# Kernel optimization log

Measured on AMD Instinct MI355X. Metric: run time of the kernel, lower is better.

Reference implementation:

```python
import jax, jax.numpy as jnp
import numpy as np

B, T, D, H = 2, 2048, 1024, 16
HD = D // H
SCALE = HD ** -0.5
NEG_INF = float(np.finfo(np.float32).min)


def setup_inputs() -> dict:
    key = jax.random.key(0)
    ks = jax.random.split(key, 10)
    s = 1.0 / np.sqrt(D)
    x = jax.random.normal(ks[0], (B, T, D), dtype=jnp.float32)
    # causal mask, True = keep, shape (B,1,T,T)
    mask = jnp.broadcast_to(jnp.tril(jnp.ones((T, T), dtype=bool)), (B, 1, T, T))
    Wq = jax.random.normal(ks[1], (D, D), dtype=jnp.float32) * s
    bq = jax.random.normal(ks[2], (D,), dtype=jnp.float32) * s
    Wk = jax.random.normal(ks[3], (D, D), dtype=jnp.float32) * s
    bk = jax.random.normal(ks[4], (D,), dtype=jnp.float32) * s
    Wv = jax.random.normal(ks[5], (D, D), dtype=jnp.float32) * s
    bv = jax.random.normal(ks[6], (D,), dtype=jnp.float32) * s
    Wo = jax.random.normal(ks[7], (D, D), dtype=jnp.float32) * s
    bo = jax.random.normal(ks[8], (D,), dtype=jnp.float32) * s
    return {"x": x, "mask": mask, "Wq": Wq, "bq": bq, "Wk": Wk, "bk": bk,
            "Wv": Wv, "bv": bv, "Wo": Wo, "bo": bo}


def _split_heads(t):
    # (B,T,D) -> (B,H,T,HD)
    return t.reshape(B, T, H, HD).transpose(0, 2, 1, 3)


def masked_rowwise_softmax(scores, mask):
    # mask: bool, True = keep; fully-masked rows return zeros.
    s = scores.astype(jnp.float32)
    masked = jnp.where(mask, s, NEG_INF)
    row_max = jnp.max(masked, axis=-1, keepdims=True)
    exps = jnp.exp(masked - row_max) * mask.astype(jnp.float32)
    denom = jnp.maximum(jnp.sum(exps, axis=-1, keepdims=True), 1e-12)
    return (exps / denom).astype(scores.dtype)


def reference(x, mask, Wq, bq, Wk, bk, Wv, bv, Wo, bo):
    q = _split_heads(x @ Wq.T + bq)
    k = _split_heads(x @ Wk.T + bk)
    v = _split_heads(x @ Wv.T + bv)
    scores = jnp.einsum('bhqd,bhkd->bhqk', q, k) * SCALE
    m = jnp.broadcast_to(mask, (B, H, T, T))
    attn = masked_rowwise_softmax(scores, m)
    y = jnp.einsum('bhqk,bhkd->bhqd', attn, v)
    y = y.transpose(0, 2, 1, 3).reshape(B, T, D)
    return y @ Wo.T + bo
```

## Files before the change

### kernel.cpp

```cpp
#include <hip/hip_runtime.h>

#define B_ 2
#define H_ 16
#define T_ 2048
#define D_ 1024
#define HD_ 64
#define NEG_HUGE (-3.402823466e38f)
#define QSCALE 0.18033688011112042f

typedef unsigned short u16;
typedef unsigned int u32;
typedef __attribute__((ext_vector_type(8))) short bf16x8;
typedef __attribute__((ext_vector_type(4))) float f32x4;
typedef __attribute__((ext_vector_type(4))) u32 u32x4;

__device__ __forceinline__ u16 f2bf(float f) {
    u32 u = __builtin_bit_cast(u32, f);
    u += 0x7FFFu + ((u >> 16) & 1u);
    return (u16)(u >> 16);
}

__device__ __forceinline__ u32 pk2bf(float f0, float f1) {
    const u32 a0 = __builtin_bit_cast(u32, f0) + 0x8000u;
    const u32 a1 = __builtin_bit_cast(u32, f1) + 0x8000u;
    return __builtin_amdgcn_perm(a1, a0, 0x07060302u);
}

__device__ __forceinline__ uint2 pk4bf(f32x4 a) {
    uint2 r;
    r.x = pk2bf(a[0], a[1]);
    r.y = pk2bf(a[2], a[3]);
    return r;
}

__device__ __forceinline__ f32x4 mfma16(bf16x8 a, bf16x8 b, f32x4 c) {
    return __builtin_amdgcn_mfma_f32_16x16x32_bf16(a, b, c, 0, 0, 0);
}

__global__ __launch_bounds__(256) void to_bf16(
    const float* __restrict__ x,  const float* __restrict__ wq,
    const float* __restrict__ wk, const float* __restrict__ wv,
    const float* __restrict__ wo, u16* __restrict__ dst)
{
    const size_t g = ((size_t)blockIdx.x * 256 + threadIdx.x) * 8;
    const float* src; size_t off;
    if      (g < (size_t)(4u << 20)) { src = x;  off = g; }
    else if (g < (size_t)(5u << 20)) { src = wq; off = g - (size_t)(4u << 20); }
    else if (g < (size_t)(6u << 20)) { src = wk; off = g - (size_t)(5u << 20); }
    else if (g < (size_t)(7u << 20)) { src = wv; off = g - (size_t)(6u << 20); }
    else                             { src = wo; off = g - (size_t)(7u << 20); }
    const float4 a = *(const float4*)&src[off];
    const float4 b = *(const float4*)&src[off + 4];
    ushort4 lo = make_ushort4(f2bf(a.x), f2bf(a.y), f2bf(a.z), f2bf(a.w));
    ushort4 hi = make_ushort4(f2bf(b.x), f2bf(b.y), f2bf(b.z), f2bf(b.w));
    *(ushort4*)&dst[g]     = lo;
    *(ushort4*)&dst[g + 4] = hi;
}

__device__ __forceinline__ void gemm128_core(
    const u16* __restrict__ P0, const u16* __restrict__ P1,
    const int m0, const int n0, u16* As, u16* Bs, f32x4 (&acc)[4][4])
{
    const int tid  = threadIdx.x;
    const int lane = tid & 63;
    const int quad = lane >> 4;
    const int l15  = lane & 15;
    const int w    = tid >> 6;
    const int wm   = (w >> 1) << 6;
    const int wn   = (w & 1) << 6;
    const int swz  = l15 & 7;

    size_t aoff[4], boff[4];
    int    loff[4];
#pragma unroll
    for (int i = 0; i < 4; ++i) {
        const int slot = i * 256 + tid;
        const int r = slot >> 3, c = slot & 7;
        const int gc = (c ^ (r & 7)) << 3;
        aoff[i] = (size_t)(m0 + r) * D_ + gc;
        boff[i] = (size_t)(n0 + r) * D_ + gc;
        loff[i] = slot * 8;
    }
    int rowA[4], rowB[4];
#pragma unroll
    for (int i = 0; i < 4; ++i) {
        rowA[i] = (wm + i * 16 + l15) * 64;
        rowB[i] = (wn + i * 16 + l15) * 64;
    }

    bf16x8 pa[4], pb[4];
#pragma unroll
    for (int i = 0; i < 4; ++i) {
        pa[i] = *(const bf16x8*)&P0[aoff[i]];
        pb[i] = *(const bf16x8*)&P1[boff[i]];
    }

    for (int k0 = 0; k0 < D_; k0 += 64) {
        __syncthreads();
#pragma unroll
        for (int i = 0; i < 4; ++i) {
            *(bf16x8*)&As[loff[i]] = pa[i];
            *(bf16x8*)&Bs[loff[i]] = pb[i];
        }
        if (k0 + 64 < D_) {
            const int kn = k0 + 64;
#pragma unroll
            for (int i = 0; i < 4; ++i) {
                pa[i] = *(const bf16x8*)&P0[aoff[i] + kn];
                pb[i] = *(const bf16x8*)&P1[boff[i] + kn];
            }
        }
        __syncthreads();
#pragma unroll
        for (int s = 0; s < 2; ++s) {
            const int ch = (((s << 2) + quad) ^ swz) << 3;
            bf16x8 am[4], bm[4];
#pragma unroll
            for (int mi = 0; mi < 4; ++mi) am[mi] = *(const bf16x8*)&As[rowA[mi] + ch];
#pragma unroll
            for (int ni = 0; ni < 4; ++ni) bm[ni] = *(const bf16x8*)&Bs[rowB[ni] + ch];
#pragma unroll
            for (int mi = 0; mi < 4; ++mi)
#pragma unroll
                for (int ni = 0; ni < 4; ++ni)
                    acc[mi][ni] = mfma16(am[mi], bm[ni], acc[mi][ni]);
        }
    }
}

__global__ __launch_bounds__(256) void gemm_qkv(
    const u16* __restrict__ xb,
    const u16* __restrict__ Wqb, const u16* __restrict__ Wkb, const u16* __restrict__ Wvb,
    const float* __restrict__ bq, const float* __restrict__ bk, const float* __restrict__ bv,
    u16* __restrict__ Qb, u16* __restrict__ Kb, u16* __restrict__ Vtb)
{
    __shared__ u16 As[128 * 64];
    __shared__ u16 Bs[128 * 64];
    const int L   = blockIdx.x;
    const int xcd = L & 7;
    const int kk  = L >> 3;
    const int tt  = (xcd << 2) + (kk & 3);
    const int ft  = (kk >> 2) & 7;
    const int z   = kk >> 5;

    f32x4 acc[4][4];
#pragma unroll
    for (int i = 0; i < 4; ++i)
#pragma unroll
        for (int j = 0; j < 4; ++j) acc[i][j] = (f32x4){0.f, 0.f, 0.f, 0.f};

    const int tid  = threadIdx.x;
    const int lane = tid & 63;
    const int quad = lane >> 4;
    const int l15  = lane & 15;
    const int w    = tid >> 6;
    const int wm   = (w >> 1) << 6;
    const int wn   = (w & 1) << 6;
    const int pq   = quad >> 1;
    const int psub = (quad & 1) << 2;

    u16* scr = ((w < 2) ? As : Bs) + ((w & 1) ? 4096 : 0);

    if (z < 2) {
        const u16*   W    = z ? Wkb : Wqb;
        const float* bias = z ? bk  : bq;
        const float  CF   = z ? 1.f : QSCALE;
        u16*         C    = z ? Kb  : Qb;
        const int m0 = ft << 7;
        const int n0 = tt << 7;
        gemm128_core(W, xb, m0, n0, As, Bs, acc);
        __syncthreads();

        const int fb = m0 + wm;
        const int h  = fb >> 6;
        const int tb = n0 + wn;
#pragma unroll
        for (int i = 0; i < 4; ++i) {
            const float4 bi = *(const float4*)&bias[fb + i * 16 + (quad << 2)];
#pragma unroll
            for (int j = 0; j < 4; ++j) {
                const int tl = j * 16 + l15;
                f32x4 a = acc[i][j];
                f32x4 v = { (a[0] + bi.x) * CF, (a[1] + bi.y) * CF,
                            (a[2] + bi.z) * CF, (a[3] + bi.w) * CF };
                *(uint2*)&scr[tl * 64 + (((2 * i + pq) ^ (tl & 7)) << 3) + psub] = pk4bf(v);
            }
        }
        __asm__ volatile("s_waitcnt lgkmcnt(0)" ::: "memory");

        const int b  = tb >> 11;
        const int t0 = tb & 2047;
#pragma unroll
        for (int e = 0; e < 8; ++e) {
            const int tl = (lane >> 3) + e * 8;
            const int c  = lane & 7;
            bf16x8 v = *(const bf16x8*)&scr[tl * 64 + ((c ^ (tl & 7)) << 3)];
            *(bf16x8*)&C[((size_t)((b << 4) + h) * T_ + t0 + tl) * HD_ + (c << 3)] = v;
        }
    } else {
        const int m0 = tt << 7;
        const int n0 = ft << 7;
        gemm128_core(xb, Wvb, m0, n0, As, Bs, acc);
        __syncthreads();

#pragma unroll
        for (int j = 0; j < 4; ++j) {
            const int row = j * 16 + l15;
            const float bi = bv[n0 + wn + row];
            const int sw = row & 7;
#pragma unroll
            for (int i = 0; i < 4; ++i) {
                f32x4 a = acc[i][j];
                f32x4 v = { a[0] + bi, a[1] + bi, a[2] + bi, a[3] + bi };
                *(uint2*)&scr[row * 64 + (((2 * i + pq) ^ sw) << 3) + psub] = pk4bf(v);
            }
        }
        __asm__ volatile("s_waitcnt lgkmcnt(0)" ::: "memory");

        const int b  = (m0 + wm) >> 11;
        const int t0 = (m0 + wm) & 2047;
        const int h  = (n0 + wn) >> 6;
#pragma unroll
        for (int e = 0; e < 8; ++e) {
            const int hdl = (lane >> 3) + e * 8;
            const int c   = lane & 7;
            bf16x8 vv = *(const bf16x8*)&scr[hdl * 64 + ((c ^ (hdl & 7)) << 3)];
            *(bf16x8*)&Vtb[((size_t)((b << 4) + h) * HD_ + hdl) * T_ + t0 + (c << 3)] = vv;
        }
    }
}

__global__ __launch_bounds__(256) void gemm_out(
    const u16* __restrict__ Ab, const u16* __restrict__ Wob,
    const float* __restrict__ bo, float* __restrict__ C)
{
    __shared__ u16 As[128 * 64];
    __shared__ u16 Bs[128 * 64];
    const int L   = blockIdx.x;
    const int xcd = L & 7;
    const int kk  = L >> 3;
    const int tt  = (xcd << 2) + (kk & 3);
    const int ft  = kk >> 2;
    const int m0  = tt << 7;
    const int n0  = ft << 7;

    f32x4 acc[4][4];
#pragma unroll
    for (int i = 0; i < 4; ++i)
#pragma unroll
        for (int j = 0; j < 4; ++j) acc[i][j] = (f32x4){0.f, 0.f, 0.f, 0.f};

    gemm128_core(Ab, Wob, m0, n0, As, Bs, acc);

    const int tid  = threadIdx.x;
    const int lane = tid & 63;
    const int quad = lane >> 4;
    const int l15  = lane & 15;
    const int w    = tid >> 6;
    const int wm   = (w >> 1) << 6;
    const int wn   = (w & 1) << 6;

    float bi[4];
#pragma unroll
    for (int ni = 0; ni < 4; ++ni) bi[ni] = bo[n0 + wn + ni * 16 + l15];

#pragma unroll
    for (int mi = 0; mi < 4; ++mi) {
        const int m = m0 + wm + mi * 16 + (quad << 2);
#pragma unroll
        for (int r = 0; r < 4; ++r)
#pragma unroll
            for (int ni = 0; ni < 4; ++ni)
                C[(size_t)(m + r) * D_ + n0 + wn + ni * 16 + l15] = acc[mi][ni][r] + bi[ni];
    }
}

__global__ __launch_bounds__(256) void attn_mfma(
    const u16* __restrict__ Qg, const u16* __restrict__ Kg,
    const u16* __restrict__ Vtg, u16* __restrict__ Out)
{
    __shared__ u16 Ks[128 * 64];
    __shared__ u16 Vs[64 * 128];
    const int tid  = threadIdx.x;
    const int w    = tid >> 6;
    const int lane = tid & 63;
    const int quad = lane >> 4;
    const int l15  = lane & 15;
    const int bh   = blockIdx.x;
    const int qt   = 31 - (int)blockIdx.y;
    const size_t base = (size_t)bh * (T_ * HD_);

    int lK[4], lV[4];
    size_t gK[4], gV[4];
#pragma unroll
    for (int i = 0; i < 4; ++i) {
        const int slot = i * 256 + tid;
        const int rk = slot >> 3, ck = slot & 7;
        lK[i] = rk * 64 + ((ck ^ (rk & 7)) << 3);
        gK[i] = base + (size_t)rk * HD_ + ck * 8;
        const int rv = slot >> 4, cv = slot & 15;
        lV[i] = rv * 128 + ((cv ^ (rv & 15)) << 3);
        gV[i] = base + (size_t)rv * T_ + cv * 8;
    }

    bf16x8 ones;
#pragma unroll
    for (int i = 0; i < 8; ++i) ones[i] = (short)0x3F80;

    const int swz7 = l15 & 7;
    const int b = bh >> 4, h = bh & 15;

    const int qloc = (w << 4) + l15;
    const int qrow = (qt << 6) + qloc;
    const bf16x8 qf0 = *(const bf16x8*)&Qg[base + (size_t)qrow * HD_ + quad * 8];
    const bf16x8 qf1 = *(const bf16x8*)&Qg[base + (size_t)qrow * HD_ + 32 + quad * 8];

    f32x4 o[4];
#pragma unroll
    for (int nt = 0; nt < 4; ++nt) o[nt] = (f32x4){0.f, 0.f, 0.f, 0.f};
    f32x4 Lacc = (f32x4){0.f, 0.f, 0.f, 0.f};

    const int nIter = (qt + 2) >> 1;
    bf16x8 kreg[4], vreg[4];
#pragma unroll
    for (int i = 0; i < 4; ++i) {
        kreg[i] = *(const bf16x8*)&Kg[gK[i]];
        vreg[i] = *(const bf16x8*)&Vtg[gV[i]];
    }

    for (int it = 0; it < nIter; ++it) {
        __syncthreads();
#pragma unroll
        for (int i = 0; i < 4; ++i) {
            *(bf16x8*)&Ks[lK[i]] = kreg[i];
            *(bf16x8*)&Vs[lV[i]] = vreg[i];
        }
        if (it + 1 < nIter) {
            const int koff = (it + 1) << 7;
#pragma unroll
            for (int i = 0; i < 4; ++i) {
                kreg[i] = *(const bf16x8*)&Kg[gK[i] + (size_t)koff * HD_];
                vreg[i] = *(const bf16x8*)&Vtg[gV[i] + koff];
            }
        }
        __syncthreads();

        f32x4 st[8];
#pragma unroll
        for (int t = 0; t < 8; ++t) {
            const int kr = (t * 16 + l15) * 64;
            const bf16x8 k0 = *(const bf16x8*)&Ks[kr + ((quad ^ swz7) << 3)];
            const bf16x8 k1 = *(const bf16x8*)&Ks[kr + (((quad + 4) ^ swz7) << 3)];
            f32x4 a = (f32x4){0.f, 0.f, 0.f, 0.f};
            a = mfma16(k0, qf0, a);
            a = mfma16(k1, qf1, a);
            st[t] = a;
        }

        if (it == nIter - 1) {
            const int koff = it << 7;
#pragma unroll
            for (int t = 0; t < 8; ++t)
#pragma unroll
                for (int r = 0; r < 4; ++r) {
                    const int kg = koff + t * 16 + (quad << 2) + r;
                    if (kg > qrow) st[t][r] = NEG_HUGE;
                }
        }

#pragma unroll
        for (int t = 0; t < 8; ++t)
#pragma unroll
            for (int r = 0; r < 4; ++r) st[t][r] = __builtin_amdgcn_exp2f(st[t][r]);

        bf16x8 pf[4];
#pragma unroll
        for (int kq = 0; kq < 4; ++kq) {
            u32 c00 = pk2bf(st[2 * kq][0],     st[2 * kq][1]);
            u32 c01 = pk2bf(st[2 * kq][2],     st[2 * kq][3]);
            u32 c10 = pk2bf(st[2 * kq + 1][0], st[2 * kq + 1][1]);
            u32 c11 = pk2bf(st[2 * kq + 1][2], st[2 * kq + 1][3]);
            asm("v_permlane32_swap_b32 %0, %1" : "+v"(c00), "+v"(c10));
            asm("v_permlane16_swap_b32 %0, %1" : "+v"(c00), "+v"(c10));
            asm("v_permlane32_swap_b32 %0, %1" : "+v"(c01), "+v"(c11));
            asm("v_permlane16_swap_b32 %0, %1" : "+v"(c01), "+v"(c11));
            u32x4 dw;
            dw[0] = c00; dw[1] = c01; dw[2] = c10; dw[3] = c11;
            pf[kq] = __builtin_bit_cast(bf16x8, dw);
        }

        __builtin_amdgcn_s_setprio(1);
#pragma unroll
        for (int nt = 0; nt < 4; ++nt) {
            f32x4 oo = o[nt];
            const int vr = (nt * 16 + l15) * 128;
#pragma unroll
            for (int kq = 0; kq < 4; ++kq) {
                const bf16x8 vf = *(const bf16x8*)&Vs[vr + ((((kq << 2) + quad) ^ l15) << 3)];
                oo = mfma16(pf[kq], vf, oo);
            }
            o[nt] = oo;
        }
#pragma unroll
        for (int kq = 0; kq < 4; ++kq)
            Lacc = mfma16(pf[kq], ones, Lacc);
        __builtin_amdgcn_s_setprio(0);
    }

    f32x4 linv;
#pragma unroll
    for (int r = 0; r < 4; ++r) linv[r] = 1.f / fmaxf(Lacc[r], 1e-30f);

#pragma unroll
    for (int nt = 0; nt < 4; ++nt)
#pragma unroll
        for (int r = 0; r < 4; ++r) {
            const int qg2 = (qt << 6) + (w << 4) + (quad << 2) + r;
            const u32 u = __builtin_bit_cast(u32, o[nt][r] * linv[r]) + 0x8000u;
            Out[(size_t)(b * T_ + qg2) * D_ + (h << 6) + nt * 16 + l15] = (u16)(u >> 16);
        }
}

extern "C" void kernel_launch(void* const* d_in, const int* in_sizes, int n_in,
                              void* d_out, int out_size, void* d_ws, size_t ws_size,
                              hipStream_t stream)
{
    const float* x  = (const float*)d_in[0];
    const float* Wq = (const float*)d_in[2];
    const float* bq = (const float*)d_in[3];
    const float* Wk = (const float*)d_in[4];
    const float* bk = (const float*)d_in[5];
    const float* Wv = (const float*)d_in[6];
    const float* bv = (const float*)d_in[7];
    const float* Wo = (const float*)d_in[8];
    const float* bo = (const float*)d_in[9];
    float* out = (float*)d_out;

    const size_t M1 = (size_t)1 << 20;
    u16* wsu = (u16*)d_ws;
    u16* xb  = wsu;
    u16* wqb = wsu + 4 * M1;
    u16* wkb = wsu + 5 * M1;
    u16* wvb = wsu + 6 * M1;
    u16* wob = wsu + 7 * M1;
    u16* Qb  = wsu + 8 * M1;
    u16* Kb  = wsu + 12 * M1;
    u16* Vtb = wsu + 16 * M1;
    u16* AOb = wsu + 20 * M1;

    to_bf16<<<4096, 256, 0, stream>>>(x, Wq, Wk, Wv, Wo, wsu);

    gemm_qkv<<<768, 256, 0, stream>>>(xb, wqb, wkb, wvb, bq, bk, bv, Qb, Kb, Vtb);

    dim3 ga(B_ * H_, T_ / 64);
    attn_mfma<<<ga, 256, 0, stream>>>(Qb, Kb, Vtb, AOb);

    gemm_out<<<256, 256, 0, stream>>>(AOb, wob, bo, out);
}
```

Measured before the change: 188.6 us.

## Rewrite QKV GEMM with 256x256 tiles, direct-to-LDS loads and double buffering

The QKV projection kernel now uses 512-thread blocks computing 256x256 output tiles (192 blocks instead of 768), with each wave owning a 128x64 sub-tile. Operands are streamed straight into LDS via global_load_lds in a two-stage double-buffered pipeline, with setprio around MFMA bursts and explicit barriers and waitcnts. The epilogues are rewritten for the wider tiles. The aim is more data reuse per byte loaded and overlap of loads with compute, at the cost of 128 KB of LDS, higher register pressure and fewer blocks than CUs, which may leave some CUs idle.

```diff
diff --git a/kernel.cpp b/kernel.cpp
--- a/kernel.cpp
+++ b/kernel.cpp
@@ -13,6 +13,9 @@
 typedef __attribute__((ext_vector_type(8))) short bf16x8;
 typedef __attribute__((ext_vector_type(4))) float f32x4;
 typedef __attribute__((ext_vector_type(4))) u32 u32x4;
+
+typedef const __attribute__((address_space(1))) void* gas_t;
+typedef __attribute__((address_space(3))) void* las_t;
 
 __device__ __forceinline__ u16 f2bf(float f) {
     u32 u = __builtin_bit_cast(u32, f);
@@ -128,104 +131,183 @@
     }
 }
 
-__global__ __launch_bounds__(256) void gemm_qkv(
+__global__ __launch_bounds__(512, 2) void gemm_qkv(
     const u16* __restrict__ xb,
     const u16* __restrict__ Wqb, const u16* __restrict__ Wkb, const u16* __restrict__ Wvb,
     const float* __restrict__ bq, const float* __restrict__ bk, const float* __restrict__ bv,
     u16* __restrict__ Qb, u16* __restrict__ Kb, u16* __restrict__ Vtb)
 {
-    __shared__ u16 As[128 * 64];
-    __shared__ u16 Bs[128 * 64];
-    const int L   = blockIdx.x;
-    const int xcd = L & 7;
-    const int kk  = L >> 3;
-    const int tt  = (xcd << 2) + (kk & 3);
-    const int ft  = (kk >> 2) & 7;
-    const int z   = kk >> 5;
-
-    f32x4 acc[4][4];
-#pragma unroll
-    for (int i = 0; i < 4; ++i)
-#pragma unroll
-        for (int j = 0; j < 4; ++j) acc[i][j] = (f32x4){0.f, 0.f, 0.f, 0.f};
-
+    __shared__ u16 lds[65536];
     const int tid  = threadIdx.x;
     const int lane = tid & 63;
     const int quad = lane >> 4;
     const int l15  = lane & 15;
     const int w    = tid >> 6;
-    const int wm   = (w >> 1) << 6;
-    const int wn   = (w & 1) << 6;
+    const int wr   = w >> 2;
+    const int wc   = w & 3;
+    const int swz7 = l15 & 7;
+
+    const int L  = blockIdx.x;
+    const int wg = (L & 7) * 24 + (L >> 3);
+    const int ftile = wg >> 4;
+    const int ttile = wg & 15;
+    const int z  = ftile >> 2;
+    const int fb = (ftile & 3) << 8;
+
+    const u16* PA; const u16* PB;
+    int Ra, Rb;
+    if (z == 0)      { PA = Wqb; PB = xb;  Ra = fb;         Rb = ttile << 8; }
+    else if (z == 1) { PA = Wkb; PB = xb;  Ra = fb;         Rb = ttile << 8; }
+    else             { PA = xb;  PB = Wvb; Ra = ttile << 8; Rb = fb;         }
+
+    const int rr  = tid >> 3;
+    const int cc8 = ((tid & 7) ^ (rr & 7)) << 3;
+    size_t srcA[4], srcB[4];
+#pragma unroll
+    for (int i = 0; i < 4; ++i) {
+        srcA[i] = (size_t)(Ra + i * 64 + rr) * D_ + cc8;
+        srcB[i] = (size_t)(Rb + i * 64 + rr) * D_ + cc8;
+    }
+    const int dstT = tid * 8;
+
+#define QKV_STAGE(p, kt) do {                                               \
+    const size_t ko_ = (size_t)(kt) * 64;                                   \
+    _Pragma("unroll")                                                       \
+    for (int i_ = 0; i_ < 4; ++i_)                                          \
+        __builtin_amdgcn_global_load_lds((gas_t)(PA + srcA[i_] + ko_),      \
+            (las_t)&lds[((p) << 14) + i_ * 4096 + dstT], 16, 0, 0);         \
+    _Pragma("unroll")                                                       \
+    for (int i_ = 0; i_ < 4; ++i_)                                          \
+        __builtin_amdgcn_global_load_lds((gas_t)(PB + srcB[i_] + ko_),      \
+            (las_t)&lds[32768 + ((p) << 14) + i_ * 4096 + dstT], 16, 0, 0); \
+} while (0)
+
+    const int baseA = ((wr << 7) + l15) * 64;
+    const int baseB = 32768 + ((wc << 6) + l15) * 64;
+    const int cs0 = (quad ^ swz7) << 3;
+    const int cs1 = ((quad + 4) ^ swz7) << 3;
+
+    f32x4 acc[8][4];
+#pragma unroll
+    for (int i = 0; i < 8; ++i)
+#pragma unroll
+        for (int j = 0; j < 4; ++j) acc[i][j] = (f32x4){0.f, 0.f, 0.f, 0.f};
+
+    QKV_STAGE(0, 0);
+    QKV_STAGE(1, 1);
+    asm volatile("s_waitcnt vmcnt(8)" ::: "memory");
+    __builtin_amdgcn_s_barrier();
+
+    for (int kt = 0; kt < 16; ++kt) {
+        const int pO = (kt & 1) << 14;
+        bf16x8 bfr[4][2], afr[4][2];
+#pragma unroll
+        for (int ni = 0; ni < 4; ++ni) {
+            bfr[ni][0] = *(const bf16x8*)&lds[pO + baseB + ni * 1024 + cs0];
+            bfr[ni][1] = *(const bf16x8*)&lds[pO + baseB + ni * 1024 + cs1];
+        }
+#pragma unroll
+        for (int mi = 0; mi < 4; ++mi) {
+            afr[mi][0] = *(const bf16x8*)&lds[pO + baseA + mi * 1024 + cs0];
+            afr[mi][1] = *(const bf16x8*)&lds[pO + baseA + mi * 1024 + cs1];
+        }
+        __builtin_amdgcn_s_setprio(1);
+#pragma unroll
+        for (int mi = 0; mi < 4; ++mi)
+#pragma unroll
+            for (int ni = 0; ni < 4; ++ni) {
+                acc[mi][ni] = mfma16(afr[mi][0], bfr[ni][0], acc[mi][ni]);
+                acc[mi][ni] = mfma16(afr[mi][1], bfr[ni][1], acc[mi][ni]);
+            }
+        __builtin_amdgcn_s_setprio(0);
+#pragma unroll
+        for (int mi = 0; mi < 4; ++mi) {
+            afr[mi][0] = *(const bf16x8*)&lds[pO + baseA + (mi + 4) * 1024 + cs0];
+            afr[mi][1] = *(const bf16x8*)&lds[pO + baseA + (mi + 4) * 1024 + cs1];
+        }
+        asm volatile("s_waitcnt lgkmcnt(0)" ::: "memory");
+        __builtin_amdgcn_sched_barrier(0);
+        __builtin_amdgcn_s_barrier();
+        __builtin_amdgcn_sched_barrier(0);
+        if (kt + 2 < 16) QKV_STAGE(kt & 1, kt + 2);
+        __builtin_amdgcn_s_setprio(1);
+#pragma unroll
+        for (int mi = 0; mi < 4; ++mi)
+#pragma unroll
+            for (int ni = 0; ni < 4; ++ni) {
+                acc[mi + 4][ni] = mfma16(afr[mi][0], bfr[ni][0], acc[mi + 4][ni]);
+                acc[mi + 4][ni] = mfma16(afr[mi][1], bfr[ni][1], acc[mi + 4][ni]);
+            }
+        __builtin_amdgcn_s_setprio(0);
+        if (kt < 14) asm volatile("s_waitcnt vmcnt(8)" ::: "memory");
+        else         asm volatile("s_waitcnt vmcnt(0)" ::: "memory");
+        __builtin_amdgcn_sched_barrier(0);
+        __builtin_amdgcn_s_barrier();
+    }
+#undef QKV_STAGE
+
+    __syncthreads();
+    u16* scr = &lds[w * 8192];
     const int pq   = quad >> 1;
     const int psub = (quad & 1) << 2;
 
-    u16* scr = ((w < 2) ? As : Bs) + ((w & 1) ? 4096 : 0);
-
     if (z < 2) {
-        const u16*   W    = z ? Wkb : Wqb;
-        const float* bias = z ? bk  : bq;
-        const float  CF   = z ? 1.f : QSCALE;
-        u16*         C    = z ? Kb  : Qb;
-        const int m0 = ft << 7;
-        const int n0 = tt << 7;
-        gemm128_core(W, xb, m0, n0, As, Bs, acc);
-        __syncthreads();
-
-        const int fb = m0 + wm;
-        const int h  = fb >> 6;
-        const int tb = n0 + wn;
-#pragma unroll
-        for (int i = 0; i < 4; ++i) {
-            const float4 bi = *(const float4*)&bias[fb + i * 16 + (quad << 2)];
-#pragma unroll
-            for (int j = 0; j < 4; ++j) {
-                const int tl = j * 16 + l15;
-                f32x4 a = acc[i][j];
+        const float* bias = (z == 0) ? bq : bk;
+        const float  CF   = (z == 0) ? QSCALE : 1.f;
+        u16*         Cq   = (z == 0) ? Qb : Kb;
+        const int fbw = fb + (wr << 7);
+        const int tbw = (ttile << 8) + (wc << 6);
+#pragma unroll
+        for (int mi = 0; mi < 8; ++mi) {
+            const float4 bi = *(const float4*)&bias[fbw + mi * 16 + (quad << 2)];
+            const int c = (mi << 1) + pq;
+#pragma unroll
+            for (int ni = 0; ni < 4; ++ni) {
+                const int tl = ni * 16 + l15;
+                f32x4 a = acc[mi][ni];
                 f32x4 v = { (a[0] + bi.x) * CF, (a[1] + bi.y) * CF,
                             (a[2] + bi.z) * CF, (a[3] + bi.w) * CF };
-                *(uint2*)&scr[tl * 64 + (((2 * i + pq) ^ (tl & 7)) << 3) + psub] = pk4bf(v);
+                *(uint2*)&scr[tl * 128 + ((c ^ (tl & 15)) << 3) + psub] = pk4bf(v);
             }
         }
         __asm__ volatile("s_waitcnt lgkmcnt(0)" ::: "memory");
-
-        const int b  = tb >> 11;
-        const int t0 = tb & 2047;
-#pragma unroll
-        for (int e = 0; e < 8; ++e) {
-            const int tl = (lane >> 3) + e * 8;
-            const int c  = lane & 7;
-            bf16x8 v = *(const bf16x8*)&scr[tl * 64 + ((c ^ (tl & 7)) << 3)];
-            *(bf16x8*)&C[((size_t)((b << 4) + h) * T_ + t0 + tl) * HD_ + (c << 3)] = v;
+        const int hb = fbw >> 6;
+#pragma unroll
+        for (int e = 0; e < 16; ++e) {
+            const int tl = (e << 2) + (lane >> 4);
+            const int c  = lane & 15;
+            bf16x8 v = *(const bf16x8*)&scr[tl * 128 + ((c ^ (tl & 15)) << 3)];
+            const int tg = tbw + tl;
+            const int bb = tg >> 11, t0 = tg & 2047;
+            *(bf16x8*)&Cq[((size_t)((bb << 4) + hb + (c >> 3)) * T_ + t0) * HD_ +
+                          ((c & 7) << 3)] = v;
         }
     } else {
-        const int m0 = tt << 7;
-        const int n0 = ft << 7;
-        gemm128_core(xb, Wvb, m0, n0, As, Bs, acc);
-        __syncthreads();
-
-#pragma unroll
-        for (int j = 0; j < 4; ++j) {
-            const int row = j * 16 + l15;
-            const float bi = bv[n0 + wn + row];
-            const int sw = row & 7;
-#pragma unroll
-            for (int i = 0; i < 4; ++i) {
-                f32x4 a = acc[i][j];
+        const int fvw = fb + (wc << 6);
+        const int h   = fvw >> 6;
+        const int tbw = (ttile << 8) + (wr << 7);
+#pragma unroll
+        for (int ni = 0; ni < 4; ++ni) {
+            const int hdrow = ni * 16 + l15;
+            const float bi = bv[fvw + ni * 16 + l15];
+            const int sw = hdrow & 15;
+#pragma unroll
+            for (int mi = 0; mi < 8; ++mi) {
+                f32x4 a = acc[mi][ni];
                 f32x4 v = { a[0] + bi, a[1] + bi, a[2] + bi, a[3] + bi };
-                *(uint2*)&scr[row * 64 + (((2 * i + pq) ^ sw) << 3) + psub] = pk4bf(v);
+                const int c = (mi << 1) + pq;
+                *(uint2*)&scr[hdrow * 128 + ((c ^ sw) << 3) + psub] = pk4bf(v);
             }
         }
         __asm__ volatile("s_waitcnt lgkmcnt(0)" ::: "memory");
-
-        const int b  = (m0 + wm) >> 11;
-        const int t0 = (m0 + wm) & 2047;
-        const int h  = (n0 + wn) >> 6;
-#pragma unroll
-        for (int e = 0; e < 8; ++e) {
-            const int hdl = (lane >> 3) + e * 8;
-            const int c   = lane & 7;
-            bf16x8 vv = *(const bf16x8*)&scr[hdl * 64 + ((c ^ (hdl & 7)) << 3)];
-            *(bf16x8*)&Vtb[((size_t)((b << 4) + h) * HD_ + hdl) * T_ + t0 + (c << 3)] = vv;
+#pragma unroll
+        for (int e = 0; e < 16; ++e) {
+            const int hdl = (e << 2) + (lane >> 4);
+            const int c   = lane & 15;
+            bf16x8 v = *(const bf16x8*)&scr[hdl * 128 + ((c ^ (hdl & 15)) << 3)];
+            const int tg = tbw + (c << 3);
+            const int bb = tg >> 11, t0 = tg & 2047;
+            *(bf16x8*)&Vtb[((size_t)((bb << 4) + h) * HD_ + hdl) * T_ + t0] = v;
         }
     }
 }
@@ -450,7 +532,7 @@
 
     to_bf16<<<4096, 256, 0, stream>>>(x, Wq, Wk, Wv, Wo, wsu);
 
-    gemm_qkv<<<768, 256, 0, stream>>>(xb, wqb, wkb, wvb, bq, bk, bv, Qb, Kb, Vtb);
+    gemm_qkv<<<192, 512, 0, stream>>>(xb, wqb, wkb, wvb, bq, bk, bv, Qb, Kb, Vtb);
 
     dim3 ga(B_ * H_, T_ / 64);
     attn_mfma<<<ga, 256, 0, stream>>>(Qb, Kb, Vtb, AOb);
```

New measurement: 186.2 us, median of 2. Within noise of the previous version (-1.3%).
